# Performance work log

Hardware: AMD Instinct MI355X
Metric: run time of the kernel (lower is better)

Reference implementation:

```python
import jax, jax.numpy as jnp
import numpy as np

D_MODEL = 1024
NUM_HEADS = 16

def setup_inputs() -> dict:
    key = jax.random.key(0)
    ks = jax.random.split(key, 5)
    std = np.sqrt(2.0 / (D_MODEL + D_MODEL))
    def w(k):
        # trunc_normal approx: normal clipped to +-3 std
        v = jax.random.truncated_normal(k, -3.0, 3.0, (D_MODEL, D_MODEL), dtype=jnp.float32) * std
        return v
    return {
        "x": jax.random.normal(ks[0], (2, 2048, D_MODEL), dtype=jnp.float32),
        "w_q": w(ks[1]),
        "w_k": w(ks[2]),
        "w_v": w(ks[3]),
        "w_o": w(ks[4]),
    }

def reference(x, w_q, w_k, w_v, w_o):
    B, S, D = x.shape
    H = NUM_HEADS
    dk = D // H
    # Linear: y = x @ W^T  (weight is [d_out, d_in])
    def proj(w):
        y = jnp.einsum('bsd,ed->bse', x, w)
        return y.reshape(B, S, H, dk).transpose(0, 2, 1, 3)  # [B,H,S,dk]
    q, k, v = proj(w_q), proj(w_k), proj(w_v)
    scale = 1.0 / jnp.sqrt(jnp.float32(dk))
    scores = jnp.einsum('bhqd,bhkd->bhqk', q, k) * scale  # [B,H,S,S]
    causal = jnp.tril(jnp.ones((S, S), dtype=bool))
    scores = jnp.where(causal, scores, -jnp.inf)
    attn = jax.nn.softmax(scores, axis=-1)
    out = jnp.einsum('bhqk,bhkd->bhqd', attn, v)  # [B,H,S,dk]
    out = out.transpose(0, 2, 1, 3).reshape(B, S, D)
    return jnp.einsum('bsd,ed->bse', out, w_o)
```

## Files before the change

### kernel.cpp

```cpp
#include <hip/hip_runtime.h>
#include <hip/hip_bf16.h>
#include <stdint.h>

#define S_LEN 2048
#define DM    1024
#define NH    16
#define DK    64
#define NBATCH 2

typedef __attribute__((ext_vector_type(8))) short bf8_t;
typedef __attribute__((ext_vector_type(4))) short s4_t;
typedef __attribute__((ext_vector_type(4))) float f4_t;

using bf16 = __hip_bfloat16;

#define NEG_BIG (-1.0e30f)
#define SCALE2  (0.125f * 1.44269504088896f)

static __device__ __forceinline__ f4_t mfma16(bf8_t a, bf8_t b, f4_t c) {
    return __builtin_amdgcn_mfma_f32_16x16x32_bf16(a, b, c, 0, 0, 0);
}

static __device__ __forceinline__ short f2b(float f) {
    __hip_bfloat16 h = __float2bfloat16(f);
    return *reinterpret_cast<short*>(&h);
}

static __device__ __forceinline__ void g2l16(const bf16* g, bf16* l) {
#if __has_builtin(__builtin_amdgcn_global_load_lds)
    __builtin_amdgcn_global_load_lds(
        (const __attribute__((address_space(1))) void*)g,
        (__attribute__((address_space(3))) void*)l, 16, 0, 0);
#else
    *(bf8_t*)l = *(const bf8_t*)g;
#endif
}

__global__ __launch_bounds__(256)
void cvt_all(const float* __restrict__ x,  const float* __restrict__ wq,
             const float* __restrict__ wk, const float* __restrict__ wv,
             const float* __restrict__ wo, bf16* __restrict__ ob) {
    const size_t SEG = 1u << 20;
    size_t i = ((size_t)blockIdx.x * 256 + threadIdx.x) * 8;
    const float* src;
    if      (i < 4 * SEG) src = x  + i;
    else if (i < 5 * SEG) src = wq + (i - 4 * SEG);
    else if (i < 6 * SEG) src = wk + (i - 5 * SEG);
    else if (i < 7 * SEG) src = wv + (i - 6 * SEG);
    else                  src = wo + (i - 7 * SEG);
    float4 f0 = *(const float4*)(src);
    float4 f1 = *(const float4*)(src + 4);
    bf8_t v;
    v[0]=f2b(f0.x); v[1]=f2b(f0.y); v[2]=f2b(f0.z); v[3]=f2b(f0.w);
    v[4]=f2b(f1.x); v[5]=f2b(f1.y); v[6]=f2b(f1.z); v[7]=f2b(f1.w);
    *(bf8_t*)(ob + i) = v;
}

#define GEMM_B_MAINLOOP(Aptr, Bptr)                                          \
    __shared__ bf16 As[128][32];                                             \
    __shared__ bf16 Bs[128][32];                                             \
    const int tid  = threadIdx.x;                                            \
    const int lane = tid & 63;                                               \
    const int w    = tid >> 6;                                               \
    const int wr   = w >> 1, wc = w & 1;                                     \
    const int lhi  = lane >> 4, llo = lane & 15;                             \
    const int bm   = blockIdx.x * 128;                                       \
    const int bn   = blockIdx.y * 128;                                       \
    const int r0c  = tid >> 2;                           \
    const int c0c  = (tid & 3) << 3;                     \
    const int r1c  = (256 + tid) >> 2;                                       \
    f4_t acc[4][4] = {};                                                     \
    for (int k0 = 0; k0 < 1024; k0 += 32) {                                  \
        __syncthreads();                                                     \
        g2l16(Aptr + (size_t)(bm + r0c) * 1024 + k0 + c0c,                   \
              &As[0][0] + (size_t)tid * 8);                                  \
        g2l16(Aptr + (size_t)(bm + r1c) * 1024 + k0 + c0c,                   \
              &As[0][0] + (size_t)(256 + tid) * 8);                          \
        g2l16(Bptr + (size_t)(bn + r0c) * 1024 + k0 + c0c,                   \
              &Bs[0][0] + (size_t)tid * 8);                                  \
        g2l16(Bptr + (size_t)(bn + r1c) * 1024 + k0 + c0c,                   \
              &Bs[0][0] + (size_t)(256 + tid) * 8);                          \
        asm volatile("s_waitcnt vmcnt(0)" ::: "memory");                     \
        __syncthreads();                                                     \
        bf8_t af[4], bfr[4];                                                 \
        _Pragma("unroll")                                                    \
        for (int i = 0; i < 4; ++i) {                                        \
            af[i]  = *(const bf8_t*)(&As[wr * 64 + i * 16 + llo][lhi * 8]);  \
            bfr[i] = *(const bf8_t*)(&Bs[wc * 64 + i * 16 + llo][lhi * 8]);  \
        }                                                                    \
        _Pragma("unroll")                                                    \
        for (int mi = 0; mi < 4; ++mi)                                       \
            _Pragma("unroll")                                                \
            for (int ni = 0; ni < 4; ++ni)                                   \
                acc[mi][ni] = mfma16(af[mi], bfr[ni], acc[mi][ni]);          \
    }

__global__ __launch_bounds__(256)
void gemm_qkv_b(const bf16* __restrict__ xb,
                const bf16* __restrict__ wqb, const bf16* __restrict__ wkb,
                const bf16* __restrict__ wvb,
                bf16* __restrict__ qws, bf16* __restrict__ kws,
                bf16* __restrict__ vtws) {
    const int z = blockIdx.z;
    const bf16* Wb = (z == 0) ? wqb : (z == 1) ? wkb : wvb;
    GEMM_B_MAINLOOP(xb, Wb)

    if (z < 2) {
        bf16* C = z ? kws : qws;
        const float sc = z ? 1.0f : SCALE2;
        #pragma unroll
        for (int mi = 0; mi < 4; ++mi)
            #pragma unroll
            for (int ni = 0; ni < 4; ++ni)
                #pragma unroll
                for (int r = 0; r < 4; ++r) {
                    int m = bm + wr * 64 + mi * 16 + lhi * 4 + r;
                    int n = bn + wc * 64 + ni * 16 + llo;
                    int b = m >> 11, s = m & (S_LEN - 1);
                    int h = n >> 6,  d = n & (DK - 1);
                    C[(((size_t)(b * NH + h) * S_LEN) + s) * DK + d] =
                        __float2bfloat16(acc[mi][ni][r] * sc);
                }
    } else {
        #pragma unroll
        for (int mi = 0; mi < 4; ++mi)
            #pragma unroll
            for (int ni = 0; ni < 4; ++ni) {
                int m0 = bm + wr * 64 + mi * 16 + lhi * 4;
                int n  = bn + wc * 64 + ni * 16 + llo;
                int b = m0 >> 11, s0 = m0 & (S_LEN - 1);
                int h = n >> 6,   d  = n & (DK - 1);
                s4_t pk;
                #pragma unroll
                for (int r = 0; r < 4; ++r) pk[r] = f2b(acc[mi][ni][r]);
                *(s4_t*)&vtws[(((size_t)(b * NH + h) * DK) + d) * S_LEN + s0] = pk;
            }
    }
}

__global__ __launch_bounds__(256)
void gemm_o_b(const bf16* __restrict__ A, const bf16* __restrict__ Wb,
              float* __restrict__ C) {
    __shared__ bf16 As[128][32];
    __shared__ bf16 Bs[64][32];
    const int tid  = threadIdx.x;
    const int lane = tid & 63;
    const int w    = tid >> 6;
    const int wr   = w >> 1, wc = w & 1;
    const int lhi  = lane >> 4, llo = lane & 15;
    const int bm   = blockIdx.x * 128;
    const int bn   = blockIdx.y * 64;
    const int r0c  = tid >> 2;
    const int c0c  = (tid & 3) << 3;
    const int r1c  = (256 + tid) >> 2;
    f4_t acc[4][2] = {};
    for (int k0 = 0; k0 < 1024; k0 += 32) {
        __syncthreads();
        g2l16(A + (size_t)(bm + r0c) * 1024 + k0 + c0c,
              &As[0][0] + (size_t)tid * 8);
        g2l16(A + (size_t)(bm + r1c) * 1024 + k0 + c0c,
              &As[0][0] + (size_t)(256 + tid) * 8);
        g2l16(Wb + (size_t)(bn + r0c) * 1024 + k0 + c0c,
              &Bs[0][0] + (size_t)tid * 8);
        asm volatile("s_waitcnt vmcnt(0)" ::: "memory");
        __syncthreads();
        bf8_t af[4], bfr[2];
        #pragma unroll
        for (int i = 0; i < 4; ++i)
            af[i] = *(const bf8_t*)(&As[wr * 64 + i * 16 + llo][lhi * 8]);
        #pragma unroll
        for (int i = 0; i < 2; ++i)
            bfr[i] = *(const bf8_t*)(&Bs[wc * 32 + i * 16 + llo][lhi * 8]);
        #pragma unroll
        for (int mi = 0; mi < 4; ++mi)
            #pragma unroll
            for (int ni = 0; ni < 2; ++ni)
                acc[mi][ni] = mfma16(af[mi], bfr[ni], acc[mi][ni]);
    }
    #pragma unroll
    for (int mi = 0; mi < 4; ++mi)
        #pragma unroll
        for (int ni = 0; ni < 2; ++ni)
            #pragma unroll
            for (int r = 0; r < 4; ++r) {
                int m = bm + wr * 64 + mi * 16 + lhi * 4 + r;
                int n = bn + wc * 32 + ni * 16 + llo;
                C[(size_t)m * DM + n] = acc[mi][ni][r];
            }
}

__global__ __launch_bounds__(256)
void gemm_qkv_f32(const float* __restrict__ x,
                  const float* __restrict__ wqp, const float* __restrict__ wkp,
                  const float* __restrict__ wvp,
                  bf16* __restrict__ qws, bf16* __restrict__ kws,
                  bf16* __restrict__ vtws) {
    constexpr int K = DM;
    constexpr int BM = 128, BK = 32, LDT = BK + 8;
    const int z = blockIdx.z;
    const float* W = (z == 0) ? wqp : (z == 1) ? wkp : wvp;
    __shared__ bf16 As[BM][LDT];
    __shared__ bf16 Bs[BM][LDT];
    const int tid  = threadIdx.x;
    const int lane = tid & 63;
    const int w    = tid >> 6;
    const int wr   = w >> 1, wc = w & 1;
    const int lhi  = lane >> 4, llo = lane & 15;
    const int bm   = blockIdx.x * BM;
    const int bn   = blockIdx.y * BM;
    f4_t acc[4][4] = {};
    for (int k0 = 0; k0 < K; k0 += BK) {
        __syncthreads();
        #pragma unroll
        for (int t = 0; t < 2; ++t) {
            int c   = t * 256 + tid;
            int row = c >> 2;
            int col = (c & 3) << 3;
            {
                const float* s0 = x + (size_t)(bm + row) * K + k0 + col;
                float4 f0 = *(const float4*)(s0);
                float4 f1 = *(const float4*)(s0 + 4);
                bf8_t a8;
                a8[0]=f2b(f0.x); a8[1]=f2b(f0.y); a8[2]=f2b(f0.z); a8[3]=f2b(f0.w);
                a8[4]=f2b(f1.x); a8[5]=f2b(f1.y); a8[6]=f2b(f1.z); a8[7]=f2b(f1.w);
                *(bf8_t*)(&As[row][col]) = a8;
            }
            {
                const float* s0 = W + (size_t)(bn + row) * K + k0 + col;
                float4 f0 = *(const float4*)(s0);
                float4 f1 = *(const float4*)(s0 + 4);
                bf8_t b8;
                b8[0]=f2b(f0.x); b8[1]=f2b(f0.y); b8[2]=f2b(f0.z); b8[3]=f2b(f0.w);
                b8[4]=f2b(f1.x); b8[5]=f2b(f1.y); b8[6]=f2b(f1.z); b8[7]=f2b(f1.w);
                *(bf8_t*)(&Bs[row][col]) = b8;
            }
        }
        __syncthreads();
        bf8_t af[4], bfr[4];
        #pragma unroll
        for (int i = 0; i < 4; ++i) {
            af[i]  = *(const bf8_t*)(&As[wr * 64 + i * 16 + llo][lhi * 8]);
            bfr[i] = *(const bf8_t*)(&Bs[wc * 64 + i * 16 + llo][lhi * 8]);
        }
        #pragma unroll
        for (int mi = 0; mi < 4; ++mi)
            #pragma unroll
            for (int ni = 0; ni < 4; ++ni)
                acc[mi][ni] = mfma16(af[mi], bfr[ni], acc[mi][ni]);
    }
    if (z < 2) {
        bf16* C = z ? kws : qws;
        const float sc = z ? 1.0f : SCALE2;
        #pragma unroll
        for (int mi = 0; mi < 4; ++mi)
            #pragma unroll
            for (int ni = 0; ni < 4; ++ni)
                #pragma unroll
                for (int r = 0; r < 4; ++r) {
                    int m = bm + wr * 64 + mi * 16 + lhi * 4 + r;
                    int n = bn + wc * 64 + ni * 16 + llo;
                    int b = m >> 11, s = m & (S_LEN - 1);
                    int h = n >> 6,  d = n & (DK - 1);
                    C[(((size_t)(b * NH + h) * S_LEN) + s) * DK + d] =
                        __float2bfloat16(acc[mi][ni][r] * sc);
                }
    } else {
        #pragma unroll
        for (int mi = 0; mi < 4; ++mi)
            #pragma unroll
            for (int ni = 0; ni < 4; ++ni) {
                int m0 = bm + wr * 64 + mi * 16 + lhi * 4;
                int n  = bn + wc * 64 + ni * 16 + llo;
                int b = m0 >> 11, s0 = m0 & (S_LEN - 1);
                int h = n >> 6,   d  = n & (DK - 1);
                s4_t pk;
                #pragma unroll
                for (int r = 0; r < 4; ++r) pk[r] = f2b(acc[mi][ni][r]);
                *(s4_t*)&vtws[(((size_t)(b * NH + h) * DK) + d) * S_LEN + s0] = pk;
            }
    }
}

__global__ __launch_bounds__(256)
void gemm_o_f32(const bf16* __restrict__ A, const float* __restrict__ W,
                float* __restrict__ C) {
    constexpr int N = DM;
    constexpr int K = DM;
    constexpr int BM = 128, BN = 64, BK = 32, LDT = BK + 8;
    __shared__ bf16 As[BM][LDT];
    __shared__ bf16 Bs[BN][LDT];
    const int tid  = threadIdx.x;
    const int lane = tid & 63;
    const int w    = tid >> 6;
    const int wr   = w >> 1, wc = w & 1;
    const int lhi  = lane >> 4, llo = lane & 15;
    const int bm   = blockIdx.x * BM;
    const int bn   = blockIdx.y * BN;
    f4_t acc[4][2] = {};
    for (int k0 = 0; k0 < K; k0 += BK) {
        __syncthreads();
        #pragma unroll
        for (int t = 0; t < 2; ++t) {
            int c   = t * 256 + tid;
            int row = c >> 2;
            int col = (c & 3) << 3;
            *(bf8_t*)(&As[row][col]) =
                *(const bf8_t*)(A + (size_t)(bm + row) * K + k0 + col);
        }
        {
            int row = tid >> 2;
            int col = (tid & 3) << 3;
            const float* s0 = W + (size_t)(bn + row) * K + k0 + col;
            float4 f0 = *(const float4*)(s0);
            float4 f1 = *(const float4*)(s0 + 4);
            bf8_t b8;
            b8[0]=f2b(f0.x); b8[1]=f2b(f0.y); b8[2]=f2b(f0.z); b8[3]=f2b(f0.w);
            b8[4]=f2b(f1.x); b8[5]=f2b(f1.y); b8[6]=f2b(f1.z); b8[7]=f2b(f1.w);
            *(bf8_t*)(&Bs[row][col]) = b8;
        }
        __syncthreads();
        bf8_t af[4], bfr[2];
        #pragma unroll
        for (int i = 0; i < 4; ++i)
            af[i] = *(const bf8_t*)(&As[wr * 64 + i * 16 + llo][lhi * 8]);
        #pragma unroll
        for (int i = 0; i < 2; ++i)
            bfr[i] = *(const bf8_t*)(&Bs[wc * 32 + i * 16 + llo][lhi * 8]);
        #pragma unroll
        for (int mi = 0; mi < 4; ++mi)
            #pragma unroll
            for (int ni = 0; ni < 2; ++ni)
                acc[mi][ni] = mfma16(af[mi], bfr[ni], acc[mi][ni]);
    }
    #pragma unroll
    for (int mi = 0; mi < 4; ++mi)
        #pragma unroll
        for (int ni = 0; ni < 2; ++ni)
            #pragma unroll
            for (int r = 0; r < 4; ++r) {
                int m = bm + wr * 64 + mi * 16 + lhi * 4 + r;
                int n = bn + wc * 32 + ni * 16 + llo;
                C[(size_t)m * N + n] = acc[mi][ni][r];
            }
}

__global__ __launch_bounds__(512, 4)
void attn_fwd(const bf16* __restrict__ Q, const bf16* __restrict__ K,
              const bf16* __restrict__ Vt, bf16* __restrict__ AO) {
    __shared__ bf16 Ks[3][64][64];
    __shared__ bf16 Vs[3][64][64];
    __shared__ bf16 Pl[8][16][72];

    const int l  = ((int)blockIdx.x & 7) * 64 + ((int)blockIdx.x >> 3);
    const int bh = l >> 4;
    const int qt = 15 - (l & 15);
    const int q0 = qt * 128;
    const int nt = 2 * qt + 2;

    const bf16* Qh = Q  + (size_t)bh * S_LEN * DK;
    const bf16* Kh = K  + (size_t)bh * S_LEN * DK;
    const bf16* Vh = Vt + (size_t)bh * DK * S_LEN;

    const int tid  = threadIdx.x;
    const int lane = tid & 63;
    const int w    = tid >> 6;
    const int lhi  = lane >> 4, llo = lane & 15;
    const int qw   = q0 + w * 16;
    const int sw   = llo & 7;

    const int srow = tid >> 3;
    const int schk = (tid & 7) ^ (srow & 7);

#define STAGE(kv, b)                                                          \
    do {                                                                      \
        g2l16(Kh + (size_t)((kv) + srow) * DK + schk * 8,                     \
              &Ks[b][0][0] + (size_t)tid * 8);                                \
        g2l16(Vh + (size_t)srow * S_LEN + (kv) + schk * 8,                    \
              &Vs[b][0][0] + (size_t)tid * 8);                                \
    } while (0)

    const bf16* qrow = Qh + (size_t)(q0 + w * 16 + llo) * DK;
    const bf8_t qf0 = *(const bf8_t*)(qrow + lhi * 8);
    const bf8_t qf1 = *(const bf8_t*)(qrow + 32 + lhi * 8);

    bf8_t ones;
    #pragma unroll
    for (int j = 0; j < 8; ++j) ones[j] = (short)0x3F80;

    STAGE(0, 0);
    STAGE(64, 1);
    asm volatile("s_waitcnt vmcnt(2)" ::: "memory");
    __builtin_amdgcn_s_barrier();

    f4_t o[4] = {};
    float lr[4] = {0.f, 0.f, 0.f, 0.f};
    float mr = NEG_BIG;

    for (int t = 0; t < nt; ++t) {
        const int kv0 = t * 64;
        const int cur = t % 3;
        const bool more = (t + 2 < nt);
        if (more) STAGE((t + 2) * 64, (t + 2) % 3);

        if (kv0 <= qw + 15) {
            f4_t s[4] = {};
            __builtin_amdgcn_s_setprio(1);
            #pragma unroll
            for (int nf = 0; nf < 4; ++nf) {
                const int R = nf * 16 + llo;
                bf8_t k0f = *(const bf8_t*)&Ks[cur][R][(lhi ^ sw) * 8];
                bf8_t k1f = *(const bf8_t*)&Ks[cur][R][((4 + lhi) ^ sw) * 8];
                s[nf] = mfma16(k0f, qf0, s[nf]);
                s[nf] = mfma16(k1f, qf1, s[nf]);
            }
            __builtin_amdgcn_s_setprio(0);

            if (kv0 + 63 > qw) {
                #pragma unroll
                for (int nf = 0; nf < 4; ++nf)
                    #pragma unroll
                    for (int r = 0; r < 4; ++r)
                        if (kv0 + nf * 16 + lhi * 4 + r > qw + llo)
                            s[nf][r] = NEG_BIG;
            }

            float pm = s[0][0];
            #pragma unroll
            for (int nf = 0; nf < 4; ++nf)
                #pragma unroll
                for (int r = 0; r < 4; ++r) pm = fmaxf(pm, s[nf][r]);
            pm = fmaxf(pm, __shfl_xor(pm, 16));
            pm = fmaxf(pm, __shfl_xor(pm, 32));

            if (__any(pm > mr + 8.0f)) {
                float mn = fmaxf(mr, pm);
                float alpha = exp2f(mr - mn);
                mr = mn;
                float ao[4];
                #pragma unroll
                for (int r = 0; r < 4; ++r) ao[r] = __shfl(alpha, lhi * 4 + r);
                #pragma unroll
                for (int df = 0; df < 4; ++df)
                    #pragma unroll
                    for (int r = 0; r < 4; ++r) o[df][r] *= ao[r];
                #pragma unroll
                for (int r = 0; r < 4; ++r) lr[r] *= ao[r];
            }

            #pragma unroll
            for (int nf = 0; nf < 4; ++nf) {
                s4_t pk;
                #pragma unroll
                for (int r = 0; r < 4; ++r) pk[r] = f2b(exp2f(s[nf][r] - mr));
                *(s4_t*)&Pl[w][llo][nf * 16 + lhi * 4] = pk;
            }

            asm volatile("s_waitcnt lgkmcnt(0)" ::: "memory");
            __builtin_amdgcn_sched_barrier(0);

            bf8_t pa0 = *(const bf8_t*)&Pl[w][llo][lhi * 8];
            bf8_t pa1 = *(const bf8_t*)&Pl[w][llo][32 + lhi * 8];

            f4_t rsacc = {};
            rsacc = mfma16(pa0, ones, rsacc);
            rsacc = mfma16(pa1, ones, rsacc);

            __builtin_amdgcn_s_setprio(1);
            #pragma unroll
            for (int df = 0; df < 4; ++df) {
                const int R = df * 16 + llo;
                bf8_t vb0 = *(const bf8_t*)&Vs[cur][R][(lhi ^ sw) * 8];
                bf8_t vb1 = *(const bf8_t*)&Vs[cur][R][((4 + lhi) ^ sw) * 8];
                o[df] = mfma16(pa0, vb0, o[df]);
                o[df] = mfma16(pa1, vb1, o[df]);
            }
            __builtin_amdgcn_s_setprio(0);

            #pragma unroll
            for (int r = 0; r < 4; ++r) lr[r] += rsacc[r];
        }

        if (more) asm volatile("s_waitcnt vmcnt(2)" ::: "memory");
        else      asm volatile("s_waitcnt vmcnt(0)" ::: "memory");
        __builtin_amdgcn_s_barrier();
    }
#undef STAGE

    const int b = bh >> 4, h = bh & (NH - 1);
    #pragma unroll
    for (int r = 0; r < 4; ++r) {
        float inv = 1.0f / lr[r];
        int q = q0 + w * 16 + lhi * 4 + r;
        bf16* orow = AO + ((size_t)(b * S_LEN + q) * DM) + h * DK;
        #pragma unroll
        for (int df = 0; df < 4; ++df)
            orow[df * 16 + llo] = __float2bfloat16(o[df][r] * inv);
    }
}

extern "C" void kernel_launch(void* const* d_in, const int* in_sizes, int n_in,
                              void* d_out, int out_size, void* d_ws, size_t ws_size,
                              hipStream_t stream) {
    const float* x  = (const float*)d_in[0];
    const float* wq = (const float*)d_in[1];
    const float* wk = (const float*)d_in[2];
    const float* wv = (const float*)d_in[3];
    const float* wo = (const float*)d_in[4];
    float* out = (float*)d_out;

    const size_t SEG   = 1u << 20;
    const size_t elems = 4 * SEG;
    const size_t need_fast = (8 * SEG + 3 * elems) * sizeof(bf16);

    dim3 blk(256);

    if (ws_size >= need_fast) {
        bf16* ob   = (bf16*)d_ws;
        bf16* xb   = ob;
        bf16* wqb  = ob + 4 * SEG;
        bf16* wkb  = ob + 5 * SEG;
        bf16* wvb  = ob + 6 * SEG;
        bf16* wob  = ob + 7 * SEG;
        bf16* qws  = ob + 8 * SEG;
        bf16* kws  = qws + elems;
        bf16* vtws = kws + elems;
        bf16* aws  = xb;

        cvt_all<<<4096, blk, 0, stream>>>(x, wq, wk, wv, wo, ob);
        gemm_qkv_b<<<dim3(32, 8, 3), blk, 0, stream>>>(xb, wqb, wkb, wvb,
                                                       qws, kws, vtws);
        attn_fwd<<<dim3(512), dim3(512), 0, stream>>>(qws, kws, vtws, aws);
        gemm_o_b<<<dim3(32, 16), blk, 0, stream>>>(aws, wob, out);
    } else {
        if (ws_size < elems * 4 * sizeof(bf16)) return;
        bf16* qws  = (bf16*)d_ws;
        bf16* kws  = qws + elems;
        bf16* vtws = kws + elems;
        bf16* aws  = vtws + elems;

        gemm_qkv_f32<<<dim3(32, 8, 3), blk, 0, stream>>>(x, wq, wk, wv,
                                                         qws, kws, vtws);
        attn_fwd<<<dim3(512), dim3(512), 0, stream>>>(qws, kws, vtws, aws);
        gemm_o_f32<<<dim3(32, 16), blk, 0, stream>>>(aws, wo, out);
    }
}
```

Before: 129.3 us.

## Permute K staging rows to keep P in registers, drop LDS round-trip

K rows are loaded into shared memory in a permuted order so the score MFMA output layout matches the A-operand layout needed for the PV MFMA. The probabilities can then be packed directly into registers instead of going through a per-warp LDS buffer with a wait. At the same time the K/V pipeline shrinks from triple to double buffering with full vmcnt(0) waits and __syncthreads each iteration. The grid also changes from a swizzled 1D schedule to a plain 2D grid, which drops the XCD-aware block remapping. Together these may expose load latency and change locality.

```diff
diff --git a/kernel.cpp b/kernel.cpp
--- a/kernel.cpp
+++ b/kernel.cpp
@@ -347,13 +347,11 @@
 __global__ __launch_bounds__(512, 4)
 void attn_fwd(const bf16* __restrict__ Q, const bf16* __restrict__ K,
               const bf16* __restrict__ Vt, bf16* __restrict__ AO) {
-    __shared__ bf16 Ks[3][64][64];
-    __shared__ bf16 Vs[3][64][64];
-    __shared__ bf16 Pl[8][16][72];
-
-    const int l  = ((int)blockIdx.x & 7) * 64 + ((int)blockIdx.x >> 3);
-    const int bh = l >> 4;
-    const int qt = 15 - (l & 15);
+    __shared__ bf16 Ks[2][64][64];
+    __shared__ bf16 Vs[2][64][64];
+
+    const int bh = blockIdx.x;
+    const int qt = 15 - (int)blockIdx.y;
     const int q0 = qt * 128;
     const int nt = 2 * qt + 2;
 
@@ -370,10 +368,12 @@
 
     const int srow = tid >> 3;
     const int schk = (tid & 7) ^ (srow & 7);
+    const int gk = (((srow >> 2) & 3) << 3) | (((srow >> 4) & 1) << 2)
+                 | (srow & 3) | ((srow >> 5) << 5);
 
 #define STAGE(kv, b)                                                          \
     do {                                                                      \
-        g2l16(Kh + (size_t)((kv) + srow) * DK + schk * 8,                     \
+        g2l16(Kh + (size_t)((kv) + gk) * DK + schk * 8,                       \
               &Ks[b][0][0] + (size_t)tid * 8);                                \
         g2l16(Vh + (size_t)srow * S_LEN + (kv) + schk * 8,                    \
               &Vs[b][0][0] + (size_t)tid * 8);                                \
@@ -388,9 +388,8 @@
     for (int j = 0; j < 8; ++j) ones[j] = (short)0x3F80;
 
     STAGE(0, 0);
-    STAGE(64, 1);
-    asm volatile("s_waitcnt vmcnt(2)" ::: "memory");
-    __builtin_amdgcn_s_barrier();
+    asm volatile("s_waitcnt vmcnt(0)" ::: "memory");
+    __syncthreads();
 
     f4_t o[4] = {};
     float lr[4] = {0.f, 0.f, 0.f, 0.f};
@@ -398,9 +397,9 @@
 
     for (int t = 0; t < nt; ++t) {
         const int kv0 = t * 64;
-        const int cur = t % 3;
-        const bool more = (t + 2 < nt);
-        if (more) STAGE((t + 2) * 64, (t + 2) % 3);
+        const int cur = t & 1;
+
+        if (t + 1 < nt) STAGE((t + 1) * 64, cur ^ 1);
 
         if (kv0 <= qw + 15) {
             f4_t s[4] = {};
@@ -420,7 +419,8 @@
                 for (int nf = 0; nf < 4; ++nf)
                     #pragma unroll
                     for (int r = 0; r < 4; ++r)
-                        if (kv0 + nf * 16 + lhi * 4 + r > qw + llo)
+                        if (kv0 + lhi * 8 + ((nf & 1) << 2) + r + ((nf >> 1) << 5)
+                            > qw + llo)
                             s[nf][r] = NEG_BIG;
             }
 
@@ -447,19 +447,14 @@
                 for (int r = 0; r < 4; ++r) lr[r] *= ao[r];
             }
 
-            #pragma unroll
-            for (int nf = 0; nf < 4; ++nf) {
-                s4_t pk;
-                #pragma unroll
-                for (int r = 0; r < 4; ++r) pk[r] = f2b(exp2f(s[nf][r] - mr));
-                *(s4_t*)&Pl[w][llo][nf * 16 + lhi * 4] = pk;
-            }
-
-            asm volatile("s_waitcnt lgkmcnt(0)" ::: "memory");
-            __builtin_amdgcn_sched_barrier(0);
-
-            bf8_t pa0 = *(const bf8_t*)&Pl[w][llo][lhi * 8];
-            bf8_t pa1 = *(const bf8_t*)&Pl[w][llo][32 + lhi * 8];
+            bf8_t pa0, pa1;
+            #pragma unroll
+            for (int r = 0; r < 4; ++r) {
+                pa0[r]     = f2b(exp2f(s[0][r] - mr));
+                pa0[4 + r] = f2b(exp2f(s[1][r] - mr));
+                pa1[r]     = f2b(exp2f(s[2][r] - mr));
+                pa1[4 + r] = f2b(exp2f(s[3][r] - mr));
+            }
 
             f4_t rsacc = {};
             rsacc = mfma16(pa0, ones, rsacc);
@@ -480,9 +475,8 @@
             for (int r = 0; r < 4; ++r) lr[r] += rsacc[r];
         }
 
-        if (more) asm volatile("s_waitcnt vmcnt(2)" ::: "memory");
-        else      asm volatile("s_waitcnt vmcnt(0)" ::: "memory");
-        __builtin_amdgcn_s_barrier();
+        asm volatile("s_waitcnt vmcnt(0)" ::: "memory");
+        __syncthreads();
     }
 #undef STAGE
 
@@ -529,7 +523,7 @@
         cvt_all<<<4096, blk, 0, stream>>>(x, wq, wk, wv, wo, ob);
         gemm_qkv_b<<<dim3(32, 8, 3), blk, 0, stream>>>(xb, wqb, wkb, wvb,
                                                        qws, kws, vtws);
-        attn_fwd<<<dim3(512), dim3(512), 0, stream>>>(qws, kws, vtws, aws);
+        attn_fwd<<<dim3(NBATCH * NH, 16), dim3(512), 0, stream>>>(qws, kws, vtws, aws);
         gemm_o_b<<<dim3(32, 16), blk, 0, stream>>>(aws, wob, out);
     } else {
         if (ws_size < elems * 4 * sizeof(bf16)) return;
@@ -540,7 +534,7 @@
 
         gemm_qkv_f32<<<dim3(32, 8, 3), blk, 0, stream>>>(x, wq, wk, wv,
                                                          qws, kws, vtws);
-        attn_fwd<<<dim3(512), dim3(512), 0, stream>>>(qws, kws, vtws, aws);
+        attn_fwd<<<dim3(NBATCH * NH, 16), dim3(512), 0, stream>>>(qws, kws, vtws, aws);
         gemm_o_f32<<<dim3(32, 16), blk, 0, stream>>>(aws, wo, out);
     }
 }
```

After: 113.4 us. 12.2% less time.
